# Performance work log

Hardware: AMD Instinct MI355X
Metric: run time of the kernel (lower is better)

## Reference

```python
import jax, jax.numpy as jnp
import numpy as np

N_SLOTS = 16
AGG_THRESHOLD = 0.5
EPS_NORM = 1e-12   # torch F.normalize eps
EPS_AGG = 1e-8


def _l2_normalize(x, axis=-1):
    n = jnp.linalg.norm(x, axis=axis, keepdims=True)
    return x / jnp.maximum(n, EPS_NORM)


def setup_inputs() -> dict:
    key = jax.random.key(0)
    B, N, D = 64, 1024, 768
    features = jax.random.normal(key, (B, N, D), dtype=jnp.float32)
    return {"features": features, "batch_size": B}


def reference(features, batch_size):
    # Greedy slot initialization, saliency_mode='norm', aggregate=True.
    B, N, D = features.shape
    features_norm = _l2_normalize(features, axis=-1)          # [B,N,D]
    saliency = jnp.linalg.norm(features, axis=-1)             # [B,N]

    def step(mask, _):
        # mask: [B,N] multiplicative suppression state
        masked_saliency = saliency * mask
        idx = jnp.argmax(masked_saliency, axis=-1)            # [B]
        selected = jnp.take_along_axis(
            features, idx[:, None, None], axis=1)[:, 0]       # [B,D]
        selected_norm = _l2_normalize(selected, axis=-1)      # [B,D]
        similarity = jnp.einsum('bnd,bd->bn', features_norm, selected_norm)
        # aggregate=True path
        agg_w = jnp.clip(similarity * mask, 0.0, None)
        agg_w = agg_w * (similarity > AGG_THRESHOLD).astype(features.dtype)
        agg_w = agg_w / (jnp.sum(agg_w, axis=-1, keepdims=True) + EPS_AGG)
        slot = jnp.einsum('bn,bnd->bd', agg_w, features)      # [B,D]
        new_mask = mask * (1.0 - jnp.clip(similarity, 0.0, 1.0))
        return new_mask, slot

    init_mask = jnp.ones((B, N), dtype=features.dtype)
    _, slots = jax.lax.scan(step, init_mask, None, length=N_SLOTS)
    return jnp.transpose(slots, (1, 0, 2))                    # [B, n_slots, D]
```

## Files before the change

kernel.cpp:

```cpp
#include <hip/hip_runtime.h>
#include <hip/hip_fp16.h>
#include <math.h>

#define B_      64
#define N_      1024
#define D_      768
#define T_      16
#define SLABS   32
#define ROWS_PB 32
#define ROWS_PW 8
#define THR     256
#define CPL     24
#define NTILE   36
#define WFG     8

typedef _Float16 half8 __attribute__((ext_vector_type(8)));
typedef float    f32x4 __attribute__((ext_vector_type(4)));

__device__ __forceinline__ float wave_sum(float v) {
    #pragma unroll
    for (int off = 32; off; off >>= 1) v += __shfl_xor(v, off);
    return v;
}
__device__ __forceinline__ float half_sum(float v) {
    #pragma unroll
    for (int off = 16; off; off >>= 1) v += __shfl_xor(v, off);
    return v;
}
__device__ __forceinline__ unsigned pack2(float a, float b) {
    __half2 h = __float22half2_rn(make_float2(a, b));
    return *(unsigned*)&h;
}
__device__ __forceinline__ void unpack8(uint4 u, float* f) {
    __half2 h; float2 q;
    h = *(__half2*)&u.x; q = __half22float2(h); f[0] = q.x; f[1] = q.y;
    h = *(__half2*)&u.y; q = __half22float2(h); f[2] = q.x; f[3] = q.y;
    h = *(__half2*)&u.z; q = __half22float2(h); f[4] = q.x; f[5] = q.y;
    h = *(__half2*)&u.w; q = __half22float2(h); f[6] = q.x; f[7] = q.y;
}

__global__ __launch_bounds__(THR)
void k_sal16v(const float* __restrict__ feat, ushort* __restrict__ f16,
              float* __restrict__ sal, float* __restrict__ rsal,
              float* __restrict__ mask, float* __restrict__ argv,
              float* __restrict__ args, int* __restrict__ argi) {
    const int blk = blockIdx.x, b = blk >> 5, g = blk & 31;
    const int tid = threadIdx.x, wave = tid >> 6, lane = tid & 63;
    const int h = lane >> 5, s = lane & 31;
    __shared__ float s_sal[ROWS_PB];

    const size_t row0 = (size_t)b * N_ + (size_t)g * ROWS_PB;
    const int r0 = wave * ROWS_PW;

    #pragma unroll
    for (int rp = 0; rp < ROWS_PW / 2; ++rp) {
        const int r = r0 + rp * 2 + h;
        const float4* fp4 = (const float4*)(feat + (row0 + r) * D_ + s * CPL);
        float4 a0 = fp4[0], a1 = fp4[1], a2 = fp4[2], a3 = fp4[3], a4 = fp4[4], a5 = fp4[5];
        uint4 w0, w1, w2;
        w0.x = pack2(a0.x, a0.y); w0.y = pack2(a0.z, a0.w);
        w0.z = pack2(a1.x, a1.y); w0.w = pack2(a1.z, a1.w);
        w1.x = pack2(a2.x, a2.y); w1.y = pack2(a2.z, a2.w);
        w1.z = pack2(a3.x, a3.y); w1.w = pack2(a3.z, a3.w);
        w2.x = pack2(a4.x, a4.y); w2.y = pack2(a4.z, a4.w);
        w2.z = pack2(a5.x, a5.y); w2.w = pack2(a5.z, a5.w);
        uint4* wp = (uint4*)(f16 + (row0 + r) * D_ + s * CPL);
        wp[0] = w0; wp[1] = w1; wp[2] = w2;

        float ss = a0.x*a0.x + a0.y*a0.y + a0.z*a0.z + a0.w*a0.w
                 + a1.x*a1.x + a1.y*a1.y + a1.z*a1.z + a1.w*a1.w
                 + a2.x*a2.x + a2.y*a2.y + a2.z*a2.z + a2.w*a2.w
                 + a3.x*a3.x + a3.y*a3.y + a3.z*a3.z + a3.w*a3.w
                 + a4.x*a4.x + a4.y*a4.y + a4.z*a4.z + a4.w*a4.w
                 + a5.x*a5.x + a5.y*a5.y + a5.z*a5.z + a5.w*a5.w;
        ss = half_sum(ss);
        if (s == 0) s_sal[r] = sqrtf(ss);
    }
    __syncthreads();

    const int rg = b * N_ + g * ROWS_PB;
    if (tid < ROWS_PB) {
        float n = s_sal[tid];
        sal[rg + tid]  = n;
        rsal[rg + tid] = 1.0f / fmaxf(n, 1e-12f);
        mask[rg + tid] = 1.0f;
    }
    if (wave == 0) {
        float v  = (lane < ROWS_PB) ? s_sal[lane] : -INFINITY;
        float sv = v;
        int   i  = (lane < ROWS_PB) ? (g * ROWS_PB + lane) : 0x7fffffff;
        #pragma unroll
        for (int off = 32; off; off >>= 1) {
            float ov = __shfl_xor(v, off);
            float osv = __shfl_xor(sv, off);
            int   oi = __shfl_xor(i, off);
            if (ov > v || (ov == v && oi < i)) { v = ov; sv = osv; i = oi; }
        }
        if (lane == 0) { argv[b*SLABS+g] = v; args[b*SLABS+g] = sv; argi[b*SLABS+g] = i; }
    }
}

__global__ __launch_bounds__(THR)
void k_gram(const ushort* __restrict__ f16, float* __restrict__ G) {
    const int bid = blockIdx.x;
    const int xcd = bid & 7, slot = bid >> 3;
    const int batch = xcd + 8 * (slot / NTILE);
    int u = slot % NTILE;
    int trow = 0, cnt = 8;
    while (u >= cnt) { u -= cnt; --cnt; ++trow; }
    const int tcol = trow + u;

    const int tid = threadIdx.x, wave = tid >> 6, lane = tid & 63;
    const int wr = wave >> 1, wc = wave & 1;

    __shared__ __align__(16) ushort lA[128 * 64];
    __shared__ __align__(16) ushort lB[128 * 64];

    const ushort* Fb = f16 + (size_t)batch * N_ * D_;
    const int row0 = trow * 128, col0 = tcol * 128;

    f32x4 acc[4][4];
    #pragma unroll
    for (int i = 0; i < 4; ++i)
        #pragma unroll
        for (int j = 0; j < 4; ++j)
            acc[i][j] = (f32x4){0.f, 0.f, 0.f, 0.f};

    for (int k0 = 0; k0 < D_; k0 += 64) {
        #pragma unroll
        for (int i = 0; i < 4; ++i) {
            const int d  = i * THR + tid;
            const int r  = d >> 3;
            const int kc = (d & 7) ^ (r & 7);
            const uint4 va = *(const uint4*)(Fb + (size_t)(row0 + r) * D_ + k0 + kc * 8);
            *(uint4*)(lA + (size_t)d * 8) = va;
            const uint4 vb = *(const uint4*)(Fb + (size_t)(col0 + r) * D_ + k0 + kc * 8);
            *(uint4*)(lB + (size_t)d * 8) = vb;
        }
        __syncthreads();

        #pragma unroll
        for (int ks = 0; ks < 2; ++ks) {
            half8 af[4], bf[4];
            #pragma unroll
            for (int fr = 0; fr < 4; ++fr) {
                const int rl = wr * 64 + fr * 16 + (lane & 15);
                const int kch = ks * 4 + (lane >> 4);
                af[fr] = *(const half8*)(lA + rl * 64 + ((kch ^ (rl & 7)) * 8));
            }
            #pragma unroll
            for (int fc = 0; fc < 4; ++fc) {
                const int cl = wc * 64 + fc * 16 + (lane & 15);
                const int kch = ks * 4 + (lane >> 4);
                bf[fc] = *(const half8*)(lB + cl * 64 + ((kch ^ (cl & 7)) * 8));
            }
            #pragma unroll
            for (int fr = 0; fr < 4; ++fr)
                #pragma unroll
                for (int fc = 0; fc < 4; ++fc)
                    acc[fr][fc] = __builtin_amdgcn_mfma_f32_16x16x32_f16(
                        af[fr], bf[fc], acc[fr][fc], 0, 0, 0);
        }
        __syncthreads();
    }

    float* Gb = G + ((size_t)batch << 20);
    #pragma unroll
    for (int fr = 0; fr < 4; ++fr) {
        #pragma unroll
        for (int fc = 0; fc < 4; ++fc) {
            const int rbase = row0 + wr * 64 + fr * 16 + (lane >> 4) * 4;
            const int c     = col0 + wc * 64 + fc * 16 + (lane & 15);
            #pragma unroll
            for (int q = 0; q < 4; ++q)
                Gb[(size_t)(rbase + q) * N_ + c] = acc[fr][fc][q];
        }
    }
}

__global__ __launch_bounds__(THR)
void k_slots(const float* __restrict__ G, const float* __restrict__ sal,
             const float* __restrict__ rsal, float* __restrict__ wbuf,
             float* __restrict__ wsum) {
    const int b = blockIdx.x, tid = threadIdx.x, wave = tid >> 6, lane = tid & 63;

    __shared__ float s_sal[N_], s_rsal[N_], s_mask[N_], s_msal[N_];
    __shared__ float s_av[4], s_wv[4];
    __shared__ int   s_ai[4];
    __shared__ int   s_idx;
    __shared__ float s_rsidx;

    #pragma unroll
    for (int k = 0; k < 4; ++k) {
        const int n = tid + k * THR;
        float sv = sal[b * N_ + n];
        s_sal[n]  = sv;
        s_rsal[n] = rsal[b * N_ + n];
        s_mask[n] = 1.0f;
        s_msal[n] = sv;
    }
    __syncthreads();

    const float* Gb = G + ((size_t)b << 20);

    for (int t = 0; t < T_; ++t) {
        {
            float v = -INFINITY; int i = 0x7fffffff;
            #pragma unroll
            for (int k = 0; k < 4; ++k) {
                const int n = tid + k * THR;
                float x = s_msal[n];
                if (x > v || (x == v && n < i)) { v = x; i = n; }
            }
            #pragma unroll
            for (int off = 32; off; off >>= 1) {
                float ov = __shfl_xor(v, off);
                int   oi = __shfl_xor(i, off);
                if (ov > v || (ov == v && oi < i)) { v = ov; i = oi; }
            }
            if (lane == 0) { s_av[wave] = v; s_ai[wave] = i; }
        }
        __syncthreads();
        if (tid == 0) {
            float v = s_av[0]; int i = s_ai[0];
            #pragma unroll
            for (int w = 1; w < 4; ++w) {
                float ov = s_av[w]; int oi = s_ai[w];
                if (ov > v || (ov == v && oi < i)) { v = ov; i = oi; }
            }
            s_idx = i;
            s_rsidx = s_rsal[i];
        }
        __syncthreads();

        const int idx = s_idx;
        const float rsi = s_rsidx;

        float wloc = 0.f;
        #pragma unroll
        for (int k = 0; k < 4; ++k) {
            const int n = tid + k * THR;
            float gv  = (n >= idx) ? Gb[(size_t)idx * N_ + n]
                                   : Gb[(size_t)n * N_ + idx];
            float sim = gv * s_rsal[n] * rsi;
            float m   = s_mask[n];
            float w   = (sim > 0.5f) ? (sim * m) : 0.f;
            float nm  = m * (1.0f - fminf(fmaxf(sim, 0.f), 1.f));
            s_mask[n] = nm;
            s_msal[n] = s_sal[n] * nm;
            wbuf[((size_t)(b * T_ + t)) * N_ + n] = w;
            wloc += w;
        }
        wloc = wave_sum(wloc);
        if (lane == 0) s_wv[wave] = wloc;
        __syncthreads();
        if (tid == 0)
            wsum[b * T_ + t] = s_wv[0] + s_wv[1] + s_wv[2] + s_wv[3];
        __syncthreads();
    }
}

__global__ __launch_bounds__(THR)
void k_wf(const ushort* __restrict__ f16, const float* __restrict__ wbuf,
          float* __restrict__ part) {
    const int bid = blockIdx.x, b = bid >> 3, rg = bid & 7;
    const int tid = threadIdx.x;
    const int RPG = N_ / WFG;

    __shared__ float s_w[T_ * (N_ / WFG)];

    for (int idx = tid; idx < T_ * RPG; idx += THR) {
        const int t = idx / RPG, r = idx % RPG;
        s_w[idx] = wbuf[((size_t)(b * T_ + t)) * N_ + rg * RPG + r];
    }
    __syncthreads();

    float acc[T_][3];
    #pragma unroll
    for (int t = 0; t < T_; ++t) { acc[t][0] = 0.f; acc[t][1] = 0.f; acc[t][2] = 0.f; }

    const _Float16* Fb = (const _Float16*)(f16 + (size_t)b * N_ * D_);
    for (int r = 0; r < RPG; ++r) {
        const _Float16* row = Fb + (size_t)(rg * RPG + r) * D_;
        const float f0 = (float)row[tid];
        const float f1 = (float)row[tid + 256];
        const float f2 = (float)row[tid + 512];
        const float* wr = s_w + r;
        #pragma unroll
        for (int t = 0; t < T_; ++t) {
            const float w = wr[t * RPG];
            acc[t][0] = fmaf(w, f0, acc[t][0]);
            acc[t][1] = fmaf(w, f1, acc[t][1]);
            acc[t][2] = fmaf(w, f2, acc[t][2]);
        }
    }

    float* pb = part + (((size_t)(b * WFG + rg)) * T_) * D_;
    #pragma unroll
    for (int t = 0; t < T_; ++t) {
        pb[(size_t)t * D_ + tid]       = acc[t][0];
        pb[(size_t)t * D_ + tid + 256] = acc[t][1];
        pb[(size_t)t * D_ + tid + 512] = acc[t][2];
    }
}

__global__ __launch_bounds__(THR)
void k_red(const float* __restrict__ part, const float* __restrict__ wsum,
           float* __restrict__ out) {
    const int bid = blockIdx.x, b = bid >> 4, t = bid & 15;
    const int tid = threadIdx.x;
    const float den = wsum[b * T_ + t] + 1e-8f;
    #pragma unroll
    for (int j = 0; j < 3; ++j) {
        const int c = tid + j * 256;
        float s = 0.f;
        #pragma unroll
        for (int rg = 0; rg < WFG; ++rg)
            s += part[(((size_t)(b * WFG + rg)) * T_ + t) * D_ + c];
        out[((size_t)(b * T_ + t)) * D_ + c] = s / den;
    }
}

__global__ __launch_bounds__(THR)
void k_fusedv(const ushort* __restrict__ f16, const float* __restrict__ sel,
              const float* __restrict__ sal, const float* __restrict__ rsal,
              float* __restrict__ mask, float* __restrict__ num,
              float* __restrict__ wsum, float* __restrict__ argv,
              float* __restrict__ args, int* __restrict__ argi) {
    const int blk = blockIdx.x, b = blk >> 5, g = blk & 31;
    const int tid = threadIdx.x, wave = tid >> 6, lane = tid & 63;
    const int h = lane >> 5, s = lane & 31;
    __shared__ __align__(16) float s_red[4 * D_];
    __shared__ float s_wsumW[4];
    __shared__ float s_msal[ROWS_PB];
    __shared__ float s_salL[ROWS_PB];
    const size_t row0 = (size_t)b * N_ + (size_t)g * ROWS_PB;
    const int rbase = b * N_ + g * ROWS_PB;
    const int r0 = wave * ROWS_PW;
    float se[CPL];
    {
        const float4* sp = (const float4*)(sel + (size_t)b * D_ + s * CPL);
        #pragma unroll
        for (int q = 0; q < 6; ++q) {
            float4 v = sp[q];
            se[q*4+0] = v.x; se[q*4+1] = v.y; se[q*4+2] = v.z; se[q*4+3] = v.w;
        }
    }
    float acc[CPL];
    #pragma unroll
    for (int i = 0; i < CPL; ++i) acc[i] = 0.f;
    float wsl = 0.f;
    #pragma unroll
    for (int rp = 0; rp < ROWS_PW / 2; ++rp) {
        const int r = r0 + rp * 2 + h;
        const uint4* dp = (const uint4*)(f16 + (row0 + r) * D_ + s * CPL);
        uint4 u0 = dp[0], u1 = dp[1], u2 = dp[2];
        float f[CPL];
        unpack8(u0, f); unpack8(u1, f + 8); unpack8(u2, f + 16);
        float dot = 0.f;
        #pragma unroll
        for (int i = 0; i < CPL; ++i) dot = fmaf(f[i], se[i], dot);
        dot = half_sum(dot);
        float rs  = rsal[rbase + r];
        float sv  = sal[rbase + r];
        float m   = mask[rbase + r];
        float sim = dot * rs;
        float wr  = (sim > 0.5f) ? (sim * m) : 0.f;
        float nm  = m * (1.0f - fminf(fmaxf(sim, 0.f), 1.f));
        if (s == 0) { mask[rbase + r] = nm; s_msal[r] = sv * nm; s_salL[r] = sv; }
        wsl += wr;
        #pragma unroll
        for (int i = 0; i < CPL; ++i) acc[i] = fmaf(wr, f[i], acc[i]);
    }
    wsl += __shfl_xor(wsl, 32);
    #pragma unroll
    for (int i = 0; i < CPL; ++i) acc[i] += __shfl_xor(acc[i], 32);
    if (h == 0) {
        float4* rw = (float4*)(s_red + wave * D_ + s * CPL);
        #pragma unroll
        for (int q = 0; q < 6; ++q) {
            float4 v;
            v.x = acc[q*4+0]; v.y = acc[q*4+1]; v.z = acc[q*4+2]; v.w = acc[q*4+3];
            rw[q] = v;
        }
    }
    if (lane == 0) s_wsumW[wave] = wsl;
    __syncthreads();
    #pragma unroll
    for (int it = 0; it < 3; ++it) {
        const int c = it * THR + tid;
        float sm = s_red[c] + s_red[D_ + c] + s_red[2*D_ + c] + s_red[3*D_ + c];
        num[((size_t)b * SLABS + g) * D_ + c] = sm;
    }
    if (tid == 0)
        wsum[b*SLABS+g] = s_wsumW[0] + s_wsumW[1] + s_wsumW[2] + s_wsumW[3];
    if (wave == 0) {
        float v  = (lane < ROWS_PB) ? s_msal[lane] : -INFINITY;
        float sv = (lane < ROWS_PB) ? s_salL[lane] : 0.f;
        int   i  = (lane < ROWS_PB) ? (g * ROWS_PB + lane) : 0x7fffffff;
        #pragma unroll
        for (int off = 32; off; off >>= 1) {
            float ov = __shfl_xor(v, off);
            float osv = __shfl_xor(sv, off);
            int   oi = __shfl_xor(i, off);
            if (ov > v || (ov == v && oi < i)) { v = ov; sv = osv; i = oi; }
        }
        if (lane == 0) { argv[b*SLABS+g] = v; args[b*SLABS+g] = sv; argi[b*SLABS+g] = i; }
    }
}

__global__ __launch_bounds__(192)
void k_out(const float* __restrict__ feat, const float* __restrict__ num,
           const float* __restrict__ wsumA, const float* __restrict__ argv,
           const float* __restrict__ args, const int* __restrict__ argi,
           float* __restrict__ sel, float* __restrict__ out, int t) {
    const int b = blockIdx.x >> 2, q = blockIdx.x & 3;
    const int tid = threadIdx.x, lane = tid & 63;
    __shared__ float s_rsel;
    __shared__ int   s_idx;
    __shared__ float s_ws;
    if (tid < 64) {
        float v  = (lane < SLABS) ? argv[b*SLABS + lane] : -INFINITY;
        float sv = (lane < SLABS) ? args[b*SLABS + lane] : 0.f;
        int   i  = (lane < SLABS) ? argi[b*SLABS + lane] : 0x7fffffff;
        float w  = (lane < SLABS) ? wsumA[b*SLABS + lane] : 0.f;
        #pragma unroll
        for (int off = 32; off; off >>= 1) {
            float ov = __shfl_xor(v, off);
            float osv = __shfl_xor(sv, off);
            int   oi = __shfl_xor(i, off);
            w += __shfl_xor(w, off);
            if (ov > v || (ov == v && oi < i)) { v = ov; sv = osv; i = oi; }
        }
        if (lane == 0) { s_idx = i; s_rsel = 1.0f / fmaxf(sv, 1e-12f); s_ws = w; }
    }
    __syncthreads();
    const int c = q * 192 + tid;
    if (t >= 0) {
        float sm = 0.f;
        #pragma unroll 8
        for (int g = 0; g < SLABS; ++g)
            sm += num[((size_t)b * SLABS + g) * D_ + c];
        out[((size_t)b * T_ + t) * D_ + c] = sm / (s_ws + 1e-8f);
    }
    sel[(size_t)b * D_ + c] = feat[((size_t)b * N_ + s_idx) * D_ + c] * s_rsel;
}

extern "C" void kernel_launch(void* const* d_in, const int* in_sizes, int n_in,
                              void* d_out, int out_size, void* d_ws, size_t ws_size,
                              hipStream_t stream) {
    const float* feat = (const float*)d_in[0];
    float* out = (float*)d_out;
    (void)in_sizes; (void)n_in; (void)out_size;

    const size_t n_sal  = (size_t)B_ * N_;
    const size_t n_arg  = (size_t)B_ * SLABS;
    const size_t n_sel  = (size_t)B_ * D_;
    const size_t n_num  = (size_t)B_ * SLABS * D_;
    const size_t n_f16  = (size_t)B_ * N_ * D_;
    const size_t n_G    = (size_t)B_ * N_ * N_;
    const size_t n_wbuf = (size_t)B_ * T_ * N_;
    const size_t n_part = (size_t)B_ * WFG * T_ * D_;

    const size_t f16_bytes = (n_f16 * sizeof(ushort) + 255) & ~(size_t)255;

    const size_t need_gram = f16_bytes
        + (n_G + n_wbuf + n_part + 3*n_sal + (size_t)B_*T_ + 3*n_arg) * sizeof(float) + 4096;
    const size_t need_mk = f16_bytes
        + (3*n_sal + 4*n_arg + n_sel + n_num) * sizeof(float) + 1024;

    if (ws_size >= need_gram) {
        char* base = (char*)d_ws;
        ushort* f16 = (ushort*)base;
        float* p = (float*)(base + f16_bytes);
        float* G     = p;        p += n_G;
        float* wbuf  = p;        p += n_wbuf;
        float* part  = p;        p += n_part;
        float* sal   = p;        p += n_sal;
        float* rsal  = p;        p += n_sal;
        float* mask  = p;        p += n_sal;
        float* wsum  = p;        p += (size_t)B_ * T_;
        float* argvD = p;        p += n_arg;
        float* argsD = p;        p += n_arg;
        int*   argiD = (int*)p;  p += n_arg;

        k_sal16v<<<B_*SLABS, THR, 0, stream>>>(feat, f16, sal, rsal, mask,
                                               argvD, argsD, argiD);
        k_gram<<<B_*NTILE, THR, 0, stream>>>(f16, G);
        k_slots<<<B_, THR, 0, stream>>>(G, sal, rsal, wbuf, wsum);
        k_wf<<<B_*WFG, THR, 0, stream>>>(f16, wbuf, part);
        k_red<<<B_*T_, THR, 0, stream>>>(part, wsum, out);
        return;
    }

    if (ws_size >= need_mk) {
        char* base = (char*)d_ws;
        ushort* f16 = (ushort*)base;
        float* p = (float*)(base + f16_bytes);
        float* sal  = p;            p += n_sal;
        float* rsal = p;            p += n_sal;
        float* mask = p;            p += n_sal;
        float* argv = p;            p += n_arg;
        float* args = p;            p += n_arg;
        int*   argi = (int*)p;      p += n_arg;
        float* wsum = p;            p += n_arg;
        float* sel  = p;            p += n_sel;
        float* num  = p;            p += n_num;

        k_sal16v<<<B_*SLABS, THR, 0, stream>>>(feat, f16, sal, rsal, mask, argv, args, argi);
        k_out<<<B_*4, 192, 0, stream>>>(feat, num, wsum, argv, args, argi, sel, out, -1);
        for (int t = 0; t < T_; ++t) {
            k_fusedv<<<B_*SLABS, THR, 0, stream>>>(f16, sel, sal, rsal, mask,
                                                   num, wsum, argv, args, argi);
            k_out<<<B_*4, 192, 0, stream>>>(feat, num, wsum, argv, args, argi, sel, out, t);
        }
        return;
    }
}
```

Measured before the change: 280.0 us.

## Use direct global-to-LDS loads in gram, share diagonal tiles, widen slots and wf kernels

The gram kernel now stages tiles with global_load_lds, which copies global memory straight into LDS without passing through registers. On diagonal tiles it loads the A tile only once and reuses it as B. The slots kernel runs 1024 threads per batch, one per token, which removes the per-thread loops and the serial argmax work. The weighted-feature kernel uses 192 threads, each doing a 4-wide fp16 vector load and a float4 store. The 1024-thread blocks may lower occupancy and add more waves to each reduction.

```diff
diff --git a/kernel.cpp b/kernel.cpp
--- a/kernel.cpp
+++ b/kernel.cpp
@@ -13,6 +13,7 @@
 #define CPL     24
 #define NTILE   36
 #define WFG     8
+#define WFTHR   192
 
 typedef _Float16 half8 __attribute__((ext_vector_type(8)));
 typedef float    f32x4 __attribute__((ext_vector_type(4)));
@@ -37,6 +38,12 @@
     h = *(__half2*)&u.y; q = __half22float2(h); f[2] = q.x; f[3] = q.y;
     h = *(__half2*)&u.z; q = __half22float2(h); f[4] = q.x; f[5] = q.y;
     h = *(__half2*)&u.w; q = __half22float2(h); f[6] = q.x; f[7] = q.y;
+}
+
+__device__ __forceinline__ void gload_lds16(const void* g, void* l) {
+    __builtin_amdgcn_global_load_lds(
+        (__attribute__((address_space(1))) void*)(g),
+        (__attribute__((address_space(3))) void*)(l), 16, 0, 0);
 }
 
 __global__ __launch_bounds__(THR)
@@ -109,6 +116,7 @@
     int trow = 0, cnt = 8;
     while (u >= cnt) { u -= cnt; --cnt; ++trow; }
     const int tcol = trow + u;
+    const bool diag = (trow == tcol);
 
     const int tid = threadIdx.x, wave = tid >> 6, lane = tid & 63;
     const int wr = wave >> 1, wc = wave & 1;
@@ -125,6 +133,8 @@
         #pragma unroll
         for (int j = 0; j < 4; ++j)
             acc[i][j] = (f32x4){0.f, 0.f, 0.f, 0.f};
+
+    const ushort* lBr = diag ? lA : lB;
 
     for (int k0 = 0; k0 < D_; k0 += 64) {
         #pragma unroll
@@ -132,10 +142,9 @@
             const int d  = i * THR + tid;
             const int r  = d >> 3;
             const int kc = (d & 7) ^ (r & 7);
-            const uint4 va = *(const uint4*)(Fb + (size_t)(row0 + r) * D_ + k0 + kc * 8);
-            *(uint4*)(lA + (size_t)d * 8) = va;
-            const uint4 vb = *(const uint4*)(Fb + (size_t)(col0 + r) * D_ + k0 + kc * 8);
-            *(uint4*)(lB + (size_t)d * 8) = vb;
+            gload_lds16(Fb + (size_t)(row0 + r) * D_ + k0 + kc * 8, lA + (size_t)d * 8);
+            if (!diag)
+                gload_lds16(Fb + (size_t)(col0 + r) * D_ + k0 + kc * 8, lB + (size_t)d * 8);
         }
         __syncthreads();
 
@@ -152,7 +161,7 @@
             for (int fc = 0; fc < 4; ++fc) {
                 const int cl = wc * 64 + fc * 16 + (lane & 15);
                 const int kch = ks * 4 + (lane >> 4);
-                bf[fc] = *(const half8*)(lB + cl * 64 + ((kch ^ (cl & 7)) * 8));
+                bf[fc] = *(const half8*)(lBr + cl * 64 + ((kch ^ (cl & 7)) * 8));
             }
             #pragma unroll
             for (int fr = 0; fr < 4; ++fr)
@@ -178,21 +187,20 @@
     }
 }
 
-__global__ __launch_bounds__(THR)
+__global__ __launch_bounds__(1024)
 void k_slots(const float* __restrict__ G, const float* __restrict__ sal,
              const float* __restrict__ rsal, float* __restrict__ wbuf,
              float* __restrict__ wsum) {
     const int b = blockIdx.x, tid = threadIdx.x, wave = tid >> 6, lane = tid & 63;
 
     __shared__ float s_sal[N_], s_rsal[N_], s_mask[N_], s_msal[N_];
-    __shared__ float s_av[4], s_wv[4];
-    __shared__ int   s_ai[4];
+    __shared__ float s_av[16], s_wv[16];
+    __shared__ int   s_ai[16];
     __shared__ int   s_idx;
     __shared__ float s_rsidx;
 
-    #pragma unroll
-    for (int k = 0; k < 4; ++k) {
-        const int n = tid + k * THR;
+    {
+        const int n = tid;
         float sv = sal[b * N_ + n];
         s_sal[n]  = sv;
         s_rsal[n] = rsal[b * N_ + n];
@@ -205,13 +213,7 @@
 
     for (int t = 0; t < T_; ++t) {
         {
-            float v = -INFINITY; int i = 0x7fffffff;
-            #pragma unroll
-            for (int k = 0; k < 4; ++k) {
-                const int n = tid + k * THR;
-                float x = s_msal[n];
-                if (x > v || (x == v && n < i)) { v = x; i = n; }
-            }
+            float v = s_msal[tid]; int i = tid;
             #pragma unroll
             for (int off = 32; off; off >>= 1) {
                 float ov = __shfl_xor(v, off);
@@ -224,7 +226,7 @@
         if (tid == 0) {
             float v = s_av[0]; int i = s_ai[0];
             #pragma unroll
-            for (int w = 1; w < 4; ++w) {
+            for (int w = 1; w < 16; ++w) {
                 float ov = s_av[w]; int oi = s_ai[w];
                 if (ov > v || (ov == v && oi < i)) { v = ov; i = oi; }
             }
@@ -236,31 +238,30 @@
         const int idx = s_idx;
         const float rsi = s_rsidx;
 
-        float wloc = 0.f;
-        #pragma unroll
-        for (int k = 0; k < 4; ++k) {
-            const int n = tid + k * THR;
-            float gv  = (n >= idx) ? Gb[(size_t)idx * N_ + n]
-                                   : Gb[(size_t)n * N_ + idx];
-            float sim = gv * s_rsal[n] * rsi;
-            float m   = s_mask[n];
-            float w   = (sim > 0.5f) ? (sim * m) : 0.f;
-            float nm  = m * (1.0f - fminf(fmaxf(sim, 0.f), 1.f));
-            s_mask[n] = nm;
-            s_msal[n] = s_sal[n] * nm;
-            wbuf[((size_t)(b * T_ + t)) * N_ + n] = w;
-            wloc += w;
-        }
-        wloc = wave_sum(wloc);
+        const int n = tid;
+        float gv  = (n >= idx) ? Gb[(size_t)idx * N_ + n]
+                               : Gb[(size_t)n * N_ + idx];
+        float sim = gv * s_rsal[n] * rsi;
+        float m   = s_mask[n];
+        float w   = (sim > 0.5f) ? (sim * m) : 0.f;
+        float nm  = m * (1.0f - fminf(fmaxf(sim, 0.f), 1.f));
+        s_mask[n] = nm;
+        s_msal[n] = s_sal[n] * nm;
+        wbuf[((size_t)(b * T_ + t)) * N_ + n] = w;
+        float wloc = wave_sum(w);
         if (lane == 0) s_wv[wave] = wloc;
         __syncthreads();
-        if (tid == 0)
-            wsum[b * T_ + t] = s_wv[0] + s_wv[1] + s_wv[2] + s_wv[3];
+        if (tid == 0) {
+            float acc = 0.f;
+            #pragma unroll
+            for (int w2 = 0; w2 < 16; ++w2) acc += s_wv[w2];
+            wsum[b * T_ + t] = acc;
+        }
         __syncthreads();
     }
 }
 
-__global__ __launch_bounds__(THR)
+__global__ __launch_bounds__(WFTHR)
 void k_wf(const ushort* __restrict__ f16, const float* __restrict__ wbuf,
           float* __restrict__ part) {
     const int bid = blockIdx.x, b = bid >> 3, rg = bid & 7;
@@ -269,38 +270,40 @@
 
     __shared__ float s_w[T_ * (N_ / WFG)];
 
-    for (int idx = tid; idx < T_ * RPG; idx += THR) {
-        const int t = idx / RPG, r = idx % RPG;
+    for (int idx = tid; idx < T_ * RPG; idx += WFTHR) {
+        const int t = idx >> 7, r = idx & 127;
         s_w[idx] = wbuf[((size_t)(b * T_ + t)) * N_ + rg * RPG + r];
     }
     __syncthreads();
 
-    float acc[T_][3];
-    #pragma unroll
-    for (int t = 0; t < T_; ++t) { acc[t][0] = 0.f; acc[t][1] = 0.f; acc[t][2] = 0.f; }
-
-    const _Float16* Fb = (const _Float16*)(f16 + (size_t)b * N_ * D_);
+    float acc[T_][4];
+    #pragma unroll
+    for (int t = 0; t < T_; ++t) {
+        acc[t][0] = 0.f; acc[t][1] = 0.f; acc[t][2] = 0.f; acc[t][3] = 0.f;
+    }
+
+    const ushort* Fb = f16 + (size_t)b * N_ * D_;
     for (int r = 0; r < RPG; ++r) {
-        const _Float16* row = Fb + (size_t)(rg * RPG + r) * D_;
-        const float f0 = (float)row[tid];
-        const float f1 = (float)row[tid + 256];
-        const float f2 = (float)row[tid + 512];
+        const uint2 u = *(const uint2*)(Fb + (size_t)(rg * RPG + r) * D_ + tid * 4);
+        __half2 h0 = *(__half2*)&u.x; float2 q0 = __half22float2(h0);
+        __half2 h1 = *(__half2*)&u.y; float2 q1 = __half22float2(h1);
+        const float f0 = q0.x, f1 = q0.y, f2 = q1.x, f3 = q1.y;
         const float* wr = s_w + r;
         #pragma unroll
         for (int t = 0; t < T_; ++t) {
-            const float w = wr[t * RPG];
+            const float w = wr[t << 7];
             acc[t][0] = fmaf(w, f0, acc[t][0]);
             acc[t][1] = fmaf(w, f1, acc[t][1]);
             acc[t][2] = fmaf(w, f2, acc[t][2]);
+            acc[t][3] = fmaf(w, f3, acc[t][3]);
         }
     }
 
     float* pb = part + (((size_t)(b * WFG + rg)) * T_) * D_;
     #pragma unroll
     for (int t = 0; t < T_; ++t) {
-        pb[(size_t)t * D_ + tid]       = acc[t][0];
-        pb[(size_t)t * D_ + tid + 256] = acc[t][1];
-        pb[(size_t)t * D_ + tid + 512] = acc[t][2];
+        float4 v; v.x = acc[t][0]; v.y = acc[t][1]; v.z = acc[t][2]; v.w = acc[t][3];
+        *(float4*)(pb + (size_t)t * D_ + tid * 4) = v;
     }
 }
 
@@ -487,8 +490,8 @@
         k_sal16v<<<B_*SLABS, THR, 0, stream>>>(feat, f16, sal, rsal, mask,
                                                argvD, argsD, argiD);
         k_gram<<<B_*NTILE, THR, 0, stream>>>(f16, G);
-        k_slots<<<B_, THR, 0, stream>>>(G, sal, rsal, wbuf, wsum);
-        k_wf<<<B_*WFG, THR, 0, stream>>>(f16, wbuf, part);
+        k_slots<<<B_, 1024, 0, stream>>>(G, sal, rsal, wbuf, wsum);
+        k_wf<<<B_*WFG, WFTHR, 0, stream>>>(f16, wbuf, part);
         k_red<<<B_*T_, THR, 0, stream>>>(part, wsum, out);
         return;
     }
```

After: 254.7 us. 9.0% less time.
